# Performance work log

Hardware: AMD Instinct MI355X
Metric: run time of the kernel (lower is better)

The kernel has to match this reference:

```python
import jax, jax.numpy as jnp
import numpy as np

N = 100000   # nodes
E = 1600000  # edges (avg degree 16), self-loops added in reference
H = 64       # hidden


def setup_inputs() -> dict:
    key = jax.random.key(0)
    k1, k2, k3, k4, k5 = jax.random.split(key, 5)
    x = jax.random.normal(k1, (N, H), dtype=jnp.float32)
    src = jax.random.randint(k2, (E,), 0, N, dtype=jnp.int32)
    off = jax.random.randint(k3, (E,), 1, N, dtype=jnp.int32)
    dst = (src + off) % N  # guaranteed no self-loops -> matches add_remaining_self_loops
    edge_index = jnp.stack([src, dst])  # row0 = j (source), row1 = i (target)
    # a_i, a_j: Linear(hidden, 1, bias=False) -> weight vectors of shape [H]
    w_i = jax.random.normal(k4, (H,), dtype=jnp.float32) / np.sqrt(H)
    w_j = jax.random.normal(k5, (H,), dtype=jnp.float32) / np.sqrt(H)
    return {"x": x, "edge_index": edge_index, "w_i": w_i, "w_j": w_j}


def reference(x, edge_index, w_i, w_j):
    n = x.shape[0]
    # add_remaining_self_loops: append (v, v) for every node (inputs have none)
    loops = jnp.arange(n, dtype=edge_index.dtype)
    src = jnp.concatenate([edge_index[0], loops])  # j
    dst = jnp.concatenate([edge_index[1], loops])  # i
    # per-node attention scalars, then per-edge gather
    s_i = x @ w_i  # [N]
    s_j = x @ w_j  # [N]
    e = jax.nn.leaky_relu(s_i[dst] + s_j[src], 0.01)  # [E+N]
    # segment softmax over destination node i (every segment non-empty via self-loop)
    e_max = jax.ops.segment_max(e, dst, num_segments=n)
    e_exp = jnp.exp(e - e_max[dst])
    denom = jax.ops.segment_sum(e_exp, dst, num_segments=n)
    alpha = e_exp / denom[dst]  # [E+N]
    # spmm: out[i] = sum_j alpha_ij * x[j], then ReLU
    out = jax.ops.segment_sum(alpha[:, None] * x[src], dst, num_segments=n)
    return jax.nn.relu(out)
```

## Files before the change

### kernel.cpp

```cpp
#include <hip/hip_runtime.h>

#define H 64
#define H4 16
#define NBUCK 196
#define CAP 9216


__global__ void gat_node_kernel(const float* __restrict__ x,
                                const float* __restrict__ w_i,
                                const float* __restrict__ w_j,
                                float* __restrict__ s_i,
                                float* __restrict__ s_j,
                                int* __restrict__ cursor,
                                int n) {
    long long gid = (long long)blockIdx.x * blockDim.x + threadIdx.x;
    if (gid < NBUCK) cursor[gid] = 0;
    int wave = (int)(gid >> 6);
    int lane = threadIdx.x & 63;
    if (wave >= n) return;

    float v = x[(long long)wave * H + lane];
    float a = v * w_i[lane];
    float b = v * w_j[lane];
    #pragma unroll
    for (int off = 32; off > 0; off >>= 1) {
        a += __shfl_down(a, off, 64);
        b += __shfl_down(b, off, 64);
    }
    if (lane == 0) {
        s_i[wave] = a;
        s_j[wave] = b;
    }
}

__global__ __launch_bounds__(1024) void gat_bin_kernel(
        const int4* __restrict__ src4, const int4* __restrict__ dst4,
        int* __restrict__ cursor, int* __restrict__ buckets, int e4) {
    __shared__ int hist[NBUCK];
    __shared__ int boff[NBUCK];
    __shared__ int boff0[NBUCK];
    __shared__ int gbase[NBUCK];
    __shared__ int wtot[4];
    __shared__ int stage[8192];
    __shared__ unsigned char sbuck[8192];

    int tid = threadIdx.x;
    if (tid < NBUCK) hist[tid] = 0;
    __syncthreads();

    int4 s[2], d[2];
    bool val[2];
    #pragma unroll
    for (int r = 0; r < 2; ++r) {
        int i4 = blockIdx.x * 2048 + r * 1024 + tid;
        val[r] = (i4 < e4);
        if (val[r]) { s[r] = src4[i4]; d[r] = dst4[i4]; }
        else        { s[r] = make_int4(0,0,0,0); d[r] = make_int4(0,0,0,0); }
    }
    #pragma unroll
    for (int r = 0; r < 2; ++r) if (val[r]) {
        atomicAdd(&hist[d[r].x >> 9], 1);
        atomicAdd(&hist[d[r].y >> 9], 1);
        atomicAdd(&hist[d[r].z >> 9], 1);
        atomicAdd(&hist[d[r].w >> 9], 1);
    }
    __syncthreads();

    if (tid < NBUCK) gbase[tid] = atomicAdd(&cursor[tid], hist[tid]);

    int v = 0, incl = 0;
    int lane = tid & 63, wv = tid >> 6;
    if (tid < 256) {
        v = (tid < NBUCK) ? hist[tid] : 0;
        incl = v;
        #pragma unroll
        for (int off = 1; off < 64; off <<= 1) {
            int t = __shfl_up(incl, off, 64);
            if (lane >= off) incl += t;
        }
        if (lane == 63) wtot[wv] = incl;
    }
    __syncthreads();
    if (tid < NBUCK) {
        int wpref = 0;
        #pragma unroll
        for (int j = 0; j < 4; ++j) wpref += (j < wv) ? wtot[j] : 0;
        int excl = wpref + incl - v;
        boff[tid]  = excl;
        boff0[tid] = excl;
    }
    __syncthreads();

    #pragma unroll
    for (int r = 0; r < 2; ++r) if (val[r]) {
        int ss[4] = {s[r].x, s[r].y, s[r].z, s[r].w};
        int dd[4] = {d[r].x, d[r].y, d[r].z, d[r].w};
        #pragma unroll
        for (int c = 0; c < 4; ++c) {
            int b = dd[c] >> 9;
            int pos = atomicAdd(&boff[b], 1);
            stage[pos] = ((dd[c] & 511) << 17) | ss[c];
            sbuck[pos] = (unsigned char)b;
        }
    }
    __syncthreads();

    int tot = boff[NBUCK - 1];
    for (int idx = tid; idx < tot; idx += 1024) {
        int b = sbuck[idx];
        buckets[b * CAP + gbase[b] + (idx - boff0[b])] = stage[idx];
    }
}

__global__ __launch_bounds__(512) void gat_sort_kernel(
        const int* __restrict__ cursor, int* __restrict__ buckets,
        int* __restrict__ row_start, int* __restrict__ count, int n) {
    __shared__ int hist[512];
    __shared__ int offs[512];
    __shared__ int stage[CAP];
    __shared__ int wtot[8];

    int b = blockIdx.x;
    int tid = threadIdx.x;
    int cnt = cursor[b];
    int* bk = buckets + b * CAP;

    hist[tid] = 0;
    __syncthreads();

    for (int i = tid; i < cnt; i += 512)
        atomicAdd(&hist[(bk[i] >> 17) & 511], 1);
    __syncthreads();

    int lane = tid & 63, wv = tid >> 6;
    int v = hist[tid];
    int incl = v;
    #pragma unroll
    for (int off = 1; off < 64; off <<= 1) {
        int t = __shfl_up(incl, off, 64);
        if (lane >= off) incl += t;
    }
    if (lane == 63) wtot[wv] = incl;
    __syncthreads();
    int wpref = 0;
    #pragma unroll
    for (int j = 0; j < 8; ++j) wpref += (j < wv) ? wtot[j] : 0;
    int excl = wpref + incl - v;
    offs[tid] = excl;
    int node = (b << 9) + tid;
    if (node < n) {
        row_start[node] = b * CAP + excl;
        count[node] = v;
    }
    __syncthreads();

    for (int i = tid; i < cnt; i += 512) {
        int w = bk[i];
        int pos = atomicAdd(&offs[(w >> 17) & 511], 1);
        stage[pos] = w & 0x1FFFF;
    }
    __syncthreads();

    for (int i = tid; i < cnt; i += 512)
        bk[i] = stage[i];
}

__global__ void gat_aggregate_kernel(const float4* __restrict__ x4,
                                     const float* __restrict__ s_i,
                                     const float* __restrict__ s_j,
                                     const int* __restrict__ row_start,
                                     const int* __restrict__ count,
                                     const int* __restrict__ csr_src,
                                     float4* __restrict__ out4, int n) {
    int node = (blockIdx.x * blockDim.x + threadIdx.x) >> 6;
    int lane = threadIdx.x & 63;
    if (node >= n) return;
    int g = lane >> 4;
    int q = lane & 15;

    float sii = s_i[node];
    int start = row_start[node];
    int cnt = count[node];

    float4 acc = make_float4(0.f, 0.f, 0.f, 0.f);
    float den = 0.f;

    for (int base = 0; base < cnt; base += 64) {
        int rem = cnt - base;
        int prsrc = node;
        if (lane < rem) prsrc = csr_src[start + base + lane];
        int m = (rem < 64) ? rem : 64;
        int mp = (m + 7) & ~7;
        for (int k = g; k < mp; k += 8) {
            int kb = k + 4;
            int s0 = __shfl(prsrc, k, 64);
            int s1 = __shfl(prsrc, kb & 63, 64);
            float sj0 = s_j[s0];
            float sj1 = s_j[s1];
            float4 xv0 = x4[(long long)s0 * H4 + q];
            float4 xv1 = x4[(long long)s1 * H4 + q];
            float e0 = sii + sj0; e0 = (e0 >= 0.f) ? e0 : 0.01f * e0;
            float e1 = sii + sj1; e1 = (e1 >= 0.f) ? e1 : 0.01f * e1;
            float w0 = (k  < m) ? __expf(e0) : 0.f;
            float w1 = (kb < m) ? __expf(e1) : 0.f;
            acc.x = fmaf(w0, xv0.x, acc.x);
            acc.y = fmaf(w0, xv0.y, acc.y);
            acc.z = fmaf(w0, xv0.z, acc.z);
            acc.w = fmaf(w0, xv0.w, acc.w);
            acc.x = fmaf(w1, xv1.x, acc.x);
            acc.y = fmaf(w1, xv1.y, acc.y);
            acc.z = fmaf(w1, xv1.z, acc.z);
            acc.w = fmaf(w1, xv1.w, acc.w);
            den += w0 + w1;
        }
    }

    #pragma unroll
    for (int off = 16; off <= 32; off <<= 1) {
        acc.x += __shfl_xor(acc.x, off, 64);
        acc.y += __shfl_xor(acc.y, off, 64);
        acc.z += __shfl_xor(acc.z, off, 64);
        acc.w += __shfl_xor(acc.w, off, 64);
        den   += __shfl_xor(den,   off, 64);
    }

    float sjn = s_j[node];
    float e0 = sii + sjn; e0 = (e0 >= 0.f) ? e0 : 0.01f * e0;
    float w0 = __expf(e0);
    float4 xv = x4[(long long)node * H4 + q];
    acc.x = fmaf(w0, xv.x, acc.x);
    acc.y = fmaf(w0, xv.y, acc.y);
    acc.z = fmaf(w0, xv.z, acc.z);
    acc.w = fmaf(w0, xv.w, acc.w);
    den += w0;

    if (lane < 16) {
        float4 o;
        float inv = 1.f / den;
        o.x = acc.x * inv; o.x = (o.x > 0.f) ? o.x : 0.f;
        o.y = acc.y * inv; o.y = (o.y > 0.f) ? o.y : 0.f;
        o.z = acc.z * inv; o.z = (o.z > 0.f) ? o.z : 0.f;
        o.w = acc.w * inv; o.w = (o.w > 0.f) ? o.w : 0.f;
        out4[(long long)node * H4 + q] = o;
    }
}

extern "C" void kernel_launch(void* const* d_in, const int* in_sizes, int n_in,
                              void* d_out, int out_size, void* d_ws, size_t ws_size,
                              hipStream_t stream) {
    const float* x    = (const float*)d_in[0];
    const int*   edge = (const int*)  d_in[1];
    const float* w_i  = (const float*)d_in[2];
    const float* w_j  = (const float*)d_in[3];

    int n     = in_sizes[0] / H;
    int e_cnt = in_sizes[1] / 2;
    const int* src = edge;
    const int* dst = edge + e_cnt;

    float* out = (float*)d_out;

    char* ws = (char*)d_ws;
    float* s_i       = (float*)ws;  ws += (size_t)n * 4;
    float* s_j       = (float*)ws;  ws += (size_t)n * 4;
    int*   cursor    = (int*)ws;    ws += 256 * 4;
    int*   row_start = (int*)ws;    ws += (size_t)n * 4;
    int*   count     = (int*)ws;    ws += (size_t)n * 4;
    int*   buckets   = (int*)ws;

    const int BLK = 256;
    int e4 = e_cnt / 4;
    int bin_blocks  = (e4 + 2047) / 2048;
    int sort_blocks = (n + 511) >> 9;

    long long node_threads = (long long)n * 64;
    gat_node_kernel<<<(unsigned)((node_threads + BLK - 1) / BLK), BLK, 0, stream>>>(
        x, w_i, w_j, s_i, s_j, cursor, n);

    gat_bin_kernel<<<bin_blocks, 1024, 0, stream>>>(
        (const int4*)src, (const int4*)dst, cursor, buckets, e4);

    gat_sort_kernel<<<sort_blocks, 512, 0, stream>>>(
        cursor, buckets, row_start, count, n);

    gat_aggregate_kernel<<<(unsigned)((node_threads + BLK - 1) / BLK), BLK, 0, stream>>>(
        (const float4*)x, s_i, s_j, row_start, count, buckets, (float4*)out, n);
}
```

Before: 176.9 us.

## Gather fp16 copy of features in aggregation; restructure bin scatter; widen sort blocks

The node kernel now also writes an fp16 copy of x, and the aggregation kernel gathers neighbour features from it, halving the bytes of the dominant random gather. The bin kernel drops its per-element bucket byte array and instead has each wave copy whole buckets contiguously to global memory. The sort kernel now runs with 1024 threads per block instead of 512. The fp16 features lose precision in the output, and the extra fp16 write adds a small cost in the node pass.

```diff
diff --git a/kernel.cpp b/kernel.cpp
--- a/kernel.cpp
+++ b/kernel.cpp
@@ -4,6 +4,8 @@
 #define H4 16
 #define NBUCK 196
 #define CAP 9216
+
+typedef _Float16 half4 __attribute__((ext_vector_type(4)));
 
 
 __global__ void gat_node_kernel(const float* __restrict__ x,
@@ -11,6 +13,7 @@
                                 const float* __restrict__ w_j,
                                 float* __restrict__ s_i,
                                 float* __restrict__ s_j,
+                                _Float16* __restrict__ xh,
                                 int* __restrict__ cursor,
                                 int n) {
     long long gid = (long long)blockIdx.x * blockDim.x + threadIdx.x;
@@ -20,6 +23,7 @@
     if (wave >= n) return;
 
     float v = x[(long long)wave * H + lane];
+    xh[(long long)wave * H + lane] = (_Float16)v;
     float a = v * w_i[lane];
     float b = v * w_j[lane];
     #pragma unroll
@@ -42,7 +46,6 @@
     __shared__ int gbase[NBUCK];
     __shared__ int wtot[4];
     __shared__ int stage[8192];
-    __shared__ unsigned char sbuck[8192];
 
     int tid = threadIdx.x;
     if (tid < NBUCK) hist[tid] = 0;
@@ -78,7 +81,7 @@
             int t = __shfl_up(incl, off, 64);
             if (lane >= off) incl += t;
         }
-        if (lane == 63) wtot[wv] = incl;
+        if (lane == 63 && wv < 4) wtot[wv] = incl;
     }
     __syncthreads();
     if (tid < NBUCK) {
@@ -100,19 +103,21 @@
             int b = dd[c] >> 9;
             int pos = atomicAdd(&boff[b], 1);
             stage[pos] = ((dd[c] & 511) << 17) | ss[c];
-            sbuck[pos] = (unsigned char)b;
-        }
-    }
-    __syncthreads();
-
-    int tot = boff[NBUCK - 1];
-    for (int idx = tid; idx < tot; idx += 1024) {
-        int b = sbuck[idx];
-        buckets[b * CAP + gbase[b] + (idx - boff0[b])] = stage[idx];
-    }
-}
-
-__global__ __launch_bounds__(512) void gat_sort_kernel(
+        }
+    }
+    __syncthreads();
+
+    for (int b = wv; b < NBUCK; b += 16) {
+        int sbase = boff0[b];
+        int L = boff[b] - sbase;
+        int gb = gbase[b];
+        int* dstp = buckets + (long long)b * CAP + gb;
+        for (int i = lane; i < L; i += 64)
+            dstp[i] = stage[sbase + i];
+    }
+}
+
+__global__ __launch_bounds__(1024) void gat_sort_kernel(
         const int* __restrict__ cursor, int* __restrict__ buckets,
         int* __restrict__ row_start, int* __restrict__ count, int n) {
     __shared__ int hist[512];
@@ -123,49 +128,52 @@
     int b = blockIdx.x;
     int tid = threadIdx.x;
     int cnt = cursor[b];
-    int* bk = buckets + b * CAP;
-
-    hist[tid] = 0;
-    __syncthreads();
-
-    for (int i = tid; i < cnt; i += 512)
+    int* bk = buckets + (long long)b * CAP;
+
+    if (tid < 512) hist[tid] = 0;
+    __syncthreads();
+
+    for (int i = tid; i < cnt; i += 1024)
         atomicAdd(&hist[(bk[i] >> 17) & 511], 1);
     __syncthreads();
 
     int lane = tid & 63, wv = tid >> 6;
-    int v = hist[tid];
+    int v = (tid < 512) ? hist[tid] : 0;
     int incl = v;
     #pragma unroll
     for (int off = 1; off < 64; off <<= 1) {
         int t = __shfl_up(incl, off, 64);
         if (lane >= off) incl += t;
     }
-    if (lane == 63) wtot[wv] = incl;
-    __syncthreads();
-    int wpref = 0;
-    #pragma unroll
-    for (int j = 0; j < 8; ++j) wpref += (j < wv) ? wtot[j] : 0;
-    int excl = wpref + incl - v;
-    offs[tid] = excl;
-    int node = (b << 9) + tid;
-    if (node < n) {
-        row_start[node] = b * CAP + excl;
-        count[node] = v;
-    }
-    __syncthreads();
-
-    for (int i = tid; i < cnt; i += 512) {
+    if (lane == 63 && wv < 8) wtot[wv] = incl;
+    __syncthreads();
+    if (tid < 512) {
+        int wpref = 0;
+        #pragma unroll
+        for (int j = 0; j < 8; ++j) wpref += (j < wv) ? wtot[j] : 0;
+        int excl = wpref + incl - v;
+        offs[tid] = excl;
+        int node = (b << 9) + tid;
+        if (node < n) {
+            row_start[node] = b * CAP + excl;
+            count[node] = v;
+        }
+    }
+    __syncthreads();
+
+    for (int i = tid; i < cnt; i += 1024) {
         int w = bk[i];
         int pos = atomicAdd(&offs[(w >> 17) & 511], 1);
         stage[pos] = w & 0x1FFFF;
     }
     __syncthreads();
 
-    for (int i = tid; i < cnt; i += 512)
+    for (int i = tid; i < cnt; i += 1024)
         bk[i] = stage[i];
 }
 
 __global__ void gat_aggregate_kernel(const float4* __restrict__ x4,
+                                     const half4* __restrict__ xh4,
                                      const float* __restrict__ s_i,
                                      const float* __restrict__ s_j,
                                      const int* __restrict__ row_start,
@@ -197,20 +205,20 @@
             int s1 = __shfl(prsrc, kb & 63, 64);
             float sj0 = s_j[s0];
             float sj1 = s_j[s1];
-            float4 xv0 = x4[(long long)s0 * H4 + q];
-            float4 xv1 = x4[(long long)s1 * H4 + q];
+            half4 hv0 = xh4[(long long)s0 * H4 + q];
+            half4 hv1 = xh4[(long long)s1 * H4 + q];
             float e0 = sii + sj0; e0 = (e0 >= 0.f) ? e0 : 0.01f * e0;
             float e1 = sii + sj1; e1 = (e1 >= 0.f) ? e1 : 0.01f * e1;
             float w0 = (k  < m) ? __expf(e0) : 0.f;
             float w1 = (kb < m) ? __expf(e1) : 0.f;
-            acc.x = fmaf(w0, xv0.x, acc.x);
-            acc.y = fmaf(w0, xv0.y, acc.y);
-            acc.z = fmaf(w0, xv0.z, acc.z);
-            acc.w = fmaf(w0, xv0.w, acc.w);
-            acc.x = fmaf(w1, xv1.x, acc.x);
-            acc.y = fmaf(w1, xv1.y, acc.y);
-            acc.z = fmaf(w1, xv1.z, acc.z);
-            acc.w = fmaf(w1, xv1.w, acc.w);
+            acc.x = fmaf(w0, (float)hv0.x, acc.x);
+            acc.y = fmaf(w0, (float)hv0.y, acc.y);
+            acc.z = fmaf(w0, (float)hv0.z, acc.z);
+            acc.w = fmaf(w0, (float)hv0.w, acc.w);
+            acc.x = fmaf(w1, (float)hv1.x, acc.x);
+            acc.y = fmaf(w1, (float)hv1.y, acc.y);
+            acc.z = fmaf(w1, (float)hv1.z, acc.z);
+            acc.w = fmaf(w1, (float)hv1.w, acc.w);
             den += w0 + w1;
         }
     }
@@ -261,12 +269,13 @@
     float* out = (float*)d_out;
 
     char* ws = (char*)d_ws;
-    float* s_i       = (float*)ws;  ws += (size_t)n * 4;
-    float* s_j       = (float*)ws;  ws += (size_t)n * 4;
-    int*   cursor    = (int*)ws;    ws += 256 * 4;
-    int*   row_start = (int*)ws;    ws += (size_t)n * 4;
-    int*   count     = (int*)ws;    ws += (size_t)n * 4;
-    int*   buckets   = (int*)ws;
+    float*    s_i       = (float*)ws;     ws += (size_t)n * 4;
+    float*    s_j       = (float*)ws;     ws += (size_t)n * 4;
+    int*      cursor    = (int*)ws;       ws += 256 * 4;
+    int*      row_start = (int*)ws;       ws += (size_t)n * 4;
+    int*      count     = (int*)ws;       ws += (size_t)n * 4;
+    int*      buckets   = (int*)ws;       ws += (size_t)NBUCK * CAP * 4;
+    _Float16* xh        = (_Float16*)ws;
 
     const int BLK = 256;
     int e4 = e_cnt / 4;
@@ -275,14 +284,15 @@
 
     long long node_threads = (long long)n * 64;
     gat_node_kernel<<<(unsigned)((node_threads + BLK - 1) / BLK), BLK, 0, stream>>>(
-        x, w_i, w_j, s_i, s_j, cursor, n);
+        x, w_i, w_j, s_i, s_j, xh, cursor, n);
 
     gat_bin_kernel<<<bin_blocks, 1024, 0, stream>>>(
         (const int4*)src, (const int4*)dst, cursor, buckets, e4);
 
-    gat_sort_kernel<<<sort_blocks, 512, 0, stream>>>(
+    gat_sort_kernel<<<sort_blocks, 1024, 0, stream>>>(
         cursor, buckets, row_start, count, n);
 
     gat_aggregate_kernel<<<(unsigned)((node_threads + BLK - 1) / BLK), BLK, 0, stream>>>(
-        (const float4*)x, s_i, s_j, row_start, count, buckets, (float4*)out, n);
-}
+        (const float4*)x, (const half4*)xh, s_i, s_j, row_start, count, buckets,
+        (float4*)out, n);
+}
```

Measured after the change: 163.6 us. 7.5% less time.
